# Optimization experiments

Measured on AMD Instinct MI355X. Metric: run time of the kernel, lower is better.

## Reference

```python
import jax, jax.numpy as jnp
import numpy as np

EOS_IDX = 2
B, LAYERS, HEADS, SEQ = 1, 33, 20, 512


def setup_inputs() -> dict:
    key = jax.random.key(0)
    k1, k2, k3, k4 = jax.random.split(key, 4)
    tokens = jax.random.randint(k1, (B, SEQ), 0, 30)
    attentions = jax.random.normal(k2, (B, LAYERS, HEADS, SEQ, SEQ), dtype=jnp.float32)
    weight = jax.random.normal(k3, (LAYERS * HEADS,), dtype=jnp.float32) * 0.05
    bias = jax.random.normal(k4, (1,), dtype=jnp.float32) * 0.05
    return {"tokens": tokens, "attentions": attentions, "weight": weight, "bias": bias}


def reference(tokens, attentions, weight, bias):
    b, nl, nh, s, _ = attentions.shape
    # mask out positions at/after EOS token pairs
    eos = (tokens != EOS_IDX).astype(attentions.dtype)           # [B, S]
    mask2d = eos[:, None, :] * eos[:, :, None]                   # [B, S, S]
    att = attentions * mask2d[:, None, None, :, :]
    # [..., :-1, :-1] then [..., 1:, 1:] == drop first and last positions
    att = att[..., 1:-1, 1:-1]                                   # [B, L, H, S-2, S-2]
    att = att.reshape(b, nl * nh, s - 2, s - 2)                  # [B, F, s2, s2]
    # symmetrize
    sym = att + jnp.swapaxes(att, -1, -2)
    # average product correction
    a1 = sym.sum(-1, keepdims=True)                              # [B, F, s2, 1]
    a2 = sym.sum(-2, keepdims=True)                              # [B, F, 1, s2]
    a12 = sym.sum((-1, -2), keepdims=True)                       # [B, F, 1, 1]
    norm = sym - a1 * a2 / a12
    logits = jnp.einsum('bfij,f->bij', norm, weight) + bias[0]
    return jax.nn.sigmoid(logits)                                # [B, s2, s2]
```

## Files before the change

kernel.cpp:

```cpp
#include <hip/hip_runtime.h>
#include <math.h>

#define SEQ   512
#define NF    660
#define CROP  510
#define EOSI  2
#define RT    16
#define NT_   32
#define NG    32

typedef float f4 __attribute__((ext_vector_type(4)));

__device__ __forceinline__ f4 ntl4(const float* p) {
    return __builtin_nontemporal_load((const f4*)p);
}

#define LOADP(buf, f, prow) do {                                              \
    const float* _b = A + ((size_t)(f) << 18) + ((size_t)(prow) << 9);        \
    buf[0] = ntl4(_b + 4 * lane);                                             \
    buf[1] = ntl4(_b + 256 + 4 * lane);                                       \
    buf[2] = ntl4(_b + 512 + 4 * lane);                                       \
    buf[3] = ntl4(_b + 768 + 4 * lane);                                       \
} while (0)

#define COMP(buf, wf, cacc, wa, POFF, f) do {                                 \
    _Pragma("unroll")                                                         \
    for (int rr = 0; rr < 2; ++rr) {                                          \
        const float mi = mrow[(POFF) * 2 + rr];                               \
        f4 x0 = buf[2 * rr], x1 = buf[2 * rr + 1];                            \
        float vals[8] = {x0[0], x0[1], x0[2], x0[3],                          \
                         x1[0], x1[1], x1[2], x1[3]};                         \
        float rs = 0.f;                                                       \
        _Pragma("unroll")                                                     \
        for (int e = 0; e < 8; ++e) {                                         \
            const float v = vals[e];                                          \
            wa[rr][e] += (wf) * v;                                            \
            rs += mskv[e] * v;                                                \
            cacc[e] += mi * v;                                                \
        }                                                                     \
        _Pragma("unroll")                                                     \
        for (int off = 32; off > 0; off >>= 1)                                \
            rs += __shfl_down(rs, off, 64);                                   \
        if (lane == 0)                                                        \
            rowsum[((size_t)(f) << 9) + row0 + (POFF) * 2 + rr] = rs;         \
    }                                                                         \
} while (0)

__global__ __launch_bounds__(256, 4) void pass1_kernel(
    const float* __restrict__ A, const int* __restrict__ tokens,
    const float* __restrict__ weight,
    float* __restrict__ WApart, float* __restrict__ rowsum, float* __restrict__ colpart)
{
    __shared__ float msk[SEQ];
    __shared__ float col_lds[2][4][2][SEQ];

    const int t = blockIdx.x, g = blockIdx.y;
    const int tid = threadIdx.x, wave = tid >> 6, lane = tid & 63;

    const int f0   = (g < 20) ? 21 * g : 420 + 20 * (g - 20);
    const int tail = (g < 20) ? 1 : 0;

    for (int j = tid; j < SEQ; j += 256)
        msk[j] = (j >= 1 && j <= SEQ - 2 && tokens[j] != EOSI) ? 1.f : 0.f;
    __syncthreads();

    float mskv[8];
    #pragma unroll
    for (int e = 0; e < 8; ++e)
        mskv[e] = msk[(e >> 2) * 256 + 4 * lane + (e & 3)];

    const int row0 = t * RT + wave * 4;
    const float mrow[4] = {msk[row0], msk[row0 + 1], msk[row0 + 2], msk[row0 + 3]};

    float waLo[2][8], waHi[2][8];
    #pragma unroll
    for (int r = 0; r < 2; ++r)
        #pragma unroll
        for (int e = 0; e < 8; ++e) { waLo[r][e] = 0.f; waHi[r][e] = 0.f; }

    f4 bufA[4], bufB[4];
    LOADP(bufA, f0, row0);

    for (int hp = 0; hp < 10; ++hp) {
        const int fa = f0 + 2 * hp, fb = fa + 1;
        const float wf0 = weight[fa], wf1 = weight[fb];
        float caccA[8] = {0, 0, 0, 0, 0, 0, 0, 0};
        float caccB[8] = {0, 0, 0, 0, 0, 0, 0, 0};

        LOADP(bufB, fa, row0 + 2);
        COMP(bufA, wf0, caccA, waLo, 0, fa);
        LOADP(bufA, fb, row0);
        COMP(bufB, wf0, caccA, waHi, 1, fa);
        LOADP(bufB, fb, row0 + 2);
        COMP(bufA, wf1, caccB, waLo, 0, fb);
        if (hp < 9)       LOADP(bufA, fa + 2, row0);
        else if (tail)    LOADP(bufA, f0 + 20, row0);
        COMP(bufB, wf1, caccB, waHi, 1, fb);

        const int pp = hp & 1;
        #pragma unroll
        for (int e = 0; e < 8; ++e) {
            const int c = (e >> 2) * 256 + 4 * lane + (e & 3);
            col_lds[pp][wave][0][c] = caccA[e];
            col_lds[pp][wave][1][c] = caccB[e];
        }
        __syncthreads();
        #pragma unroll
        for (int jj = 0; jj < 4; ++jj) {
            const int j = jj * 256 + tid;
            const int h = j >> 9, c = j & 511;
            colpart[((size_t)t * NF + fa + h) * SEQ + c] =
                col_lds[pp][0][h][c] + col_lds[pp][1][h][c]
              + col_lds[pp][2][h][c] + col_lds[pp][3][h][c];
        }
    }

    if (tail) {
        const int ft = f0 + 20;
        const float wft = weight[ft];
        float caccA[8] = {0, 0, 0, 0, 0, 0, 0, 0};
        LOADP(bufB, ft, row0 + 2);
        COMP(bufA, wft, caccA, waLo, 0, ft);
        COMP(bufB, wft, caccA, waHi, 1, ft);
        #pragma unroll
        for (int e = 0; e < 8; ++e)
            col_lds[0][wave][0][(e >> 2) * 256 + 4 * lane + (e & 3)] = caccA[e];
        __syncthreads();
        #pragma unroll
        for (int jj = 0; jj < 2; ++jj) {
            const int c = jj * 256 + tid;
            colpart[((size_t)t * NF + ft) * SEQ + c] =
                col_lds[0][0][0][c] + col_lds[0][1][0][c]
              + col_lds[0][2][0][c] + col_lds[0][3][0][c];
        }
    }

    float* __restrict__ wp = WApart + (size_t)g * SEQ * SEQ;
    #pragma unroll
    for (int rr = 0; rr < 2; ++rr) {
        f4 l0 = {waLo[rr][0], waLo[rr][1], waLo[rr][2], waLo[rr][3]};
        f4 l1 = {waLo[rr][4], waLo[rr][5], waLo[rr][6], waLo[rr][7]};
        *(f4*)(wp + ((size_t)(row0 + rr) << 9) + 4 * lane) = l0;
        *(f4*)(wp + ((size_t)(row0 + rr) << 9) + 256 + 4 * lane) = l1;
        f4 h0 = {waHi[rr][0], waHi[rr][1], waHi[rr][2], waHi[rr][3]};
        f4 h1 = {waHi[rr][4], waHi[rr][5], waHi[rr][6], waHi[rr][7]};
        *(f4*)(wp + ((size_t)(row0 + 2 + rr) << 9) + 4 * lane) = h0;
        *(f4*)(wp + ((size_t)(row0 + 2 + rr) << 9) + 256 + 4 * lane) = h1;
    }
}

__global__ __launch_bounds__(512) void kernel2(
    const float* __restrict__ WApart, float* __restrict__ WA,
    const float* __restrict__ rowsum, const float* __restrict__ colpart,
    const int* __restrict__ tokens, const float* __restrict__ weight,
    float* __restrict__ a1, float* __restrict__ sfac)
{
    __shared__ float part[8];
    const int b = blockIdx.x, tid = threadIdx.x;
    if (b < 128) {
        const size_t idx4 = (size_t)b * 512 + tid;
        f4 a = ntl4(WApart + 4 * idx4);
        #pragma unroll
        for (int g = 1; g < NG; ++g) {
            f4 x = ntl4(WApart + (size_t)g * (SEQ * SEQ) + 4 * idx4);
            a += x;
        }
        *(f4*)(WA + 4 * idx4) = a;
    } else {
        const int f = b - 128, j = tid;
        float cs = 0.f;
        #pragma unroll
        for (int t = 0; t < NT_; ++t)
            cs += colpart[((size_t)t * NF + f) * SEQ + j];
        const float m = (j >= 1 && j <= SEQ - 2 && tokens[j] != EOSI) ? 1.f : 0.f;
        const float v = m * (rowsum[((size_t)f << 9) + j] + cs);
        a1[((size_t)f << 9) + j] = v;
        float s = v;
        #pragma unroll
        for (int off = 32; off > 0; off >>= 1)
            s += __shfl_down(s, off, 64);
        const int wave = tid >> 6, lane = tid & 63;
        if (lane == 0) part[wave] = s;
        __syncthreads();
        if (tid == 0) {
            float a12 = 0.f;
            #pragma unroll
            for (int k = 0; k < 8; ++k) a12 += part[k];
            sfac[f] = weight[f] / a12;
        }
    }
}

__global__ __launch_bounds__(256) void pass3_kernel(
    const float* __restrict__ WA, const float* __restrict__ a1,
    const float* __restrict__ sfac, const int* __restrict__ tokens,
    const float* __restrict__ bias, float* __restrict__ out)
{
    const int TI = blockIdx.y * 16;
    const int TJ = blockIdx.x * 16;
    const int tid = threadIdx.x;
    const int tx = tid & 15, ty = tid >> 4;

    __shared__ float u_s[32][17];
    __shared__ float v_s[32][17];

    float acc = 0.f;

    for (int f0 = 0; f0 < NF; f0 += 32) {
        #pragma unroll
        for (int c = 0; c < 4; ++c) {
            const int e = c * 256 + tid;
            const int arr = e >> 9, ff = (e >> 4) & 31, ii = e & 15;
            const int f = f0 + ff;
            float val = 0.f;
            if (f < NF) {
                if (arr == 0) {
                    int Iu = TI + 1 + ii; if (Iu > SEQ - 1) Iu = SEQ - 1;
                    val = a1[((size_t)f << 9) + Iu] * sfac[f];
                } else {
                    int Ju = TJ + 1 + ii; if (Ju > SEQ - 1) Ju = SEQ - 1;
                    val = a1[((size_t)f << 9) + Ju];
                }
            }
            if (arr == 0) u_s[ff][ii] = val; else v_s[ff][ii] = val;
        }
        __syncthreads();
        #pragma unroll
        for (int ff = 0; ff < 32; ++ff)
            acc += u_s[ff][ty] * v_s[ff][tx];
        __syncthreads();
    }

    const int i = TI + ty, j = TJ + tx;
    if (i < CROP && j < CROP) {
        const int I = i + 1, J = j + 1;
        const float mi = (tokens[I] != EOSI) ? 1.f : 0.f;
        const float mj = (tokens[J] != EOSI) ? 1.f : 0.f;
        const float first = mi * mj * (WA[((size_t)I << 9) + J] + WA[((size_t)J << 9) + I]);
        const float logit = first - acc + bias[0];
        out[(size_t)i * CROP + j] = 1.f / (1.f + expf(-logit));
    }
}

extern "C" void kernel_launch(void* const* d_in, const int* in_sizes, int n_in,
                              void* d_out, int out_size, void* d_ws, size_t ws_size,
                              hipStream_t stream) {
    const int*   tokens = (const int*)d_in[0];
    const float* A      = (const float*)d_in[1];
    const float* weight = (const float*)d_in[2];
    const float* bias   = (const float*)d_in[3];
    float* out = (float*)d_out;

    float* WApart  = (float*)d_ws;
    float* colpart = WApart + (size_t)NG * SEQ * SEQ;
    float* WA      = colpart + (size_t)NT_ * NF * SEQ;
    float* rowsum  = WA + (size_t)SEQ * SEQ;
    float* a1      = rowsum + (size_t)NF * SEQ;
    float* sfac    = a1 + (size_t)NF * SEQ;

    dim3 g1(NT_, NG);
    pass1_kernel<<<g1, 256, 0, stream>>>(A, tokens, weight, WApart, rowsum, colpart);

    kernel2<<<128 + NF, 512, 0, stream>>>(WApart, WA, rowsum, colpart, tokens, weight, a1, sfac);

    dim3 g3(32, 32);
    pass3_kernel<<<g3, 256, 0, stream>>>(WA, a1, sfac, tokens, bias, out);
}
```

Baseline: 249.1 us.

## Split features into 33 uniform groups of 20 and drop nontemporal loads

Feature groups are repartitioned from 32 uneven groups (21/20 features) into 33 groups of 20, which removes the tail-feature path and means one more WApart partial to reduce in kernel2. Nontemporal loads are replaced with plain vector loads, __syncthreads is swapped for an inline lgkmcnt wait plus s_barrier, and the column-partial write is vectorised to float2. The occupancy hint in launch bounds is dropped and the reduction loops in kernel2 are only partially unrolled. The host launch grid must change to 33 groups; that part is not visible here.

```diff
diff --git a/kernel.cpp b/kernel.cpp
--- a/kernel.cpp
+++ b/kernel.cpp
@@ -6,21 +6,21 @@
 #define CROP  510
 #define EOSI  2
 #define RT    16
+#define GH    20
 #define NT_   32
-#define NG    32
+#define NG    33
 
 typedef float f4 __attribute__((ext_vector_type(4)));
-
-__device__ __forceinline__ f4 ntl4(const float* p) {
-    return __builtin_nontemporal_load((const f4*)p);
-}
+typedef float f2 __attribute__((ext_vector_type(2)));
+
+#define BARRIER_LGKM() asm volatile("s_waitcnt lgkmcnt(0)\n\ts_barrier" ::: "memory")
 
 #define LOADP(buf, f, prow) do {                                              \
     const float* _b = A + ((size_t)(f) << 18) + ((size_t)(prow) << 9);        \
-    buf[0] = ntl4(_b + 4 * lane);                                             \
-    buf[1] = ntl4(_b + 256 + 4 * lane);                                       \
-    buf[2] = ntl4(_b + 512 + 4 * lane);                                       \
-    buf[3] = ntl4(_b + 768 + 4 * lane);                                       \
+    buf[0] = *(const f4*)(_b + 4 * lane);                                     \
+    buf[1] = *(const f4*)(_b + 256 + 4 * lane);                               \
+    buf[2] = *(const f4*)(_b + 512 + 4 * lane);                               \
+    buf[3] = *(const f4*)(_b + 768 + 4 * lane);                               \
 } while (0)
 
 #define COMP(buf, wf, cacc, wa, POFF, f) do {                                 \
@@ -46,7 +46,7 @@
     }                                                                         \
 } while (0)
 
-__global__ __launch_bounds__(256, 4) void pass1_kernel(
+__global__ __launch_bounds__(256) void pass1_kernel(
     const float* __restrict__ A, const int* __restrict__ tokens,
     const float* __restrict__ weight,
     float* __restrict__ WApart, float* __restrict__ rowsum, float* __restrict__ colpart)
@@ -57,12 +57,9 @@
     const int t = blockIdx.x, g = blockIdx.y;
     const int tid = threadIdx.x, wave = tid >> 6, lane = tid & 63;
 
-    const int f0   = (g < 20) ? 21 * g : 420 + 20 * (g - 20);
-    const int tail = (g < 20) ? 1 : 0;
-
     for (int j = tid; j < SEQ; j += 256)
         msk[j] = (j >= 1 && j <= SEQ - 2 && tokens[j] != EOSI) ? 1.f : 0.f;
-    __syncthreads();
+    BARRIER_LGKM();
 
     float mskv[8];
     #pragma unroll
@@ -79,10 +76,11 @@
         for (int e = 0; e < 8; ++e) { waLo[r][e] = 0.f; waHi[r][e] = 0.f; }
 
     f4 bufA[4], bufB[4];
-    LOADP(bufA, f0, row0);
+    const int fbase = g * GH;
+    LOADP(bufA, fbase, row0);
 
     for (int hp = 0; hp < 10; ++hp) {
-        const int fa = f0 + 2 * hp, fb = fa + 1;
+        const int fa = fbase + 2 * hp, fb = fa + 1;
         const float wf0 = weight[fa], wf1 = weight[fb];
         float caccA[8] = {0, 0, 0, 0, 0, 0, 0, 0};
         float caccB[8] = {0, 0, 0, 0, 0, 0, 0, 0};
@@ -93,8 +91,7 @@
         COMP(bufB, wf0, caccA, waHi, 1, fa);
         LOADP(bufB, fb, row0 + 2);
         COMP(bufA, wf1, caccB, waLo, 0, fb);
-        if (hp < 9)       LOADP(bufA, fa + 2, row0);
-        else if (tail)    LOADP(bufA, f0 + 20, row0);
+        if (hp < 9) LOADP(bufA, fa + 2, row0);
         COMP(bufB, wf1, caccB, waHi, 1, fb);
 
         const int pp = hp & 1;
@@ -104,34 +101,16 @@
             col_lds[pp][wave][0][c] = caccA[e];
             col_lds[pp][wave][1][c] = caccB[e];
         }
-        __syncthreads();
-        #pragma unroll
-        for (int jj = 0; jj < 4; ++jj) {
-            const int j = jj * 256 + tid;
-            const int h = j >> 9, c = j & 511;
-            colpart[((size_t)t * NF + fa + h) * SEQ + c] =
-                col_lds[pp][0][h][c] + col_lds[pp][1][h][c]
-              + col_lds[pp][2][h][c] + col_lds[pp][3][h][c];
-        }
-    }
-
-    if (tail) {
-        const int ft = f0 + 20;
-        const float wft = weight[ft];
-        float caccA[8] = {0, 0, 0, 0, 0, 0, 0, 0};
-        LOADP(bufB, ft, row0 + 2);
-        COMP(bufA, wft, caccA, waLo, 0, ft);
-        COMP(bufB, wft, caccA, waHi, 1, ft);
-        #pragma unroll
-        for (int e = 0; e < 8; ++e)
-            col_lds[0][wave][0][(e >> 2) * 256 + 4 * lane + (e & 3)] = caccA[e];
-        __syncthreads();
-        #pragma unroll
-        for (int jj = 0; jj < 2; ++jj) {
-            const int c = jj * 256 + tid;
-            colpart[((size_t)t * NF + ft) * SEQ + c] =
-                col_lds[0][0][0][c] + col_lds[0][1][0][c]
-              + col_lds[0][2][0][c] + col_lds[0][3][0][c];
+        BARRIER_LGKM();
+        #pragma unroll
+        for (int h = 0; h < 2; ++h) {
+            const int c = 2 * tid;
+            f2 s;
+            s[0] = col_lds[pp][0][h][c]     + col_lds[pp][1][h][c]
+                 + col_lds[pp][2][h][c]     + col_lds[pp][3][h][c];
+            s[1] = col_lds[pp][0][h][c + 1] + col_lds[pp][1][h][c + 1]
+                 + col_lds[pp][2][h][c + 1] + col_lds[pp][3][h][c + 1];
+            *(f2*)(colpart + ((size_t)t * NF + fa + h) * SEQ + c) = s;
         }
     }
 
@@ -159,17 +138,17 @@
     const int b = blockIdx.x, tid = threadIdx.x;
     if (b < 128) {
         const size_t idx4 = (size_t)b * 512 + tid;
-        f4 a = ntl4(WApart + 4 * idx4);
-        #pragma unroll
+        f4 a = *(const f4*)(WApart + 4 * idx4);
+        #pragma unroll 8
         for (int g = 1; g < NG; ++g) {
-            f4 x = ntl4(WApart + (size_t)g * (SEQ * SEQ) + 4 * idx4);
+            f4 x = *(const f4*)(WApart + (size_t)g * (SEQ * SEQ) + 4 * idx4);
             a += x;
         }
         *(f4*)(WA + 4 * idx4) = a;
     } else {
         const int f = b - 128, j = tid;
         float cs = 0.f;
-        #pragma unroll
+        #pragma unroll 8
         for (int t = 0; t < NT_; ++t)
             cs += colpart[((size_t)t * NF + f) * SEQ + j];
         const float m = (j >= 1 && j <= SEQ - 2 && tokens[j] != EOSI) ? 1.f : 0.f;
```

Result: faster. 220.6 us (-11.4%).
